# Optimization experiments

Measured on AMD Instinct MI355X. Metric: run time of the kernel, lower is better.

Reference implementation:

```python
import jax, jax.numpy as jnp
import numpy as np

E = 96   # embed dim (MultiheadAttention(96, 6))
H = 6    # heads
DH = E // H  # head dim = 16


def setup_inputs() -> dict:
    key = jax.random.key(0)
    ks = jax.random.split(key, 6)
    N, G = 4096, 64
    feats = jax.random.normal(ks[0], (N, E), jnp.float32)
    group = jax.random.randint(ks[1], (N,), 0, G)
    s = 1.0 / np.sqrt(E)
    # nn.MultiheadAttention packed in_proj [3E, E] and out_proj [E, E]
    w_in = jax.random.uniform(ks[2], (3 * E, E), jnp.float32, -s, s)
    b_in = jnp.zeros((3 * E,), jnp.float32)
    w_out = jax.random.uniform(ks[3], (E, E), jnp.float32, -s, s)
    b_out = jnp.zeros((E,), jnp.float32)
    # classifier Linear(96, 1)
    w_cls = jax.random.uniform(ks[4], (1, E), jnp.float32, -s, s)
    b_cls = jnp.zeros((1,), jnp.float32)
    return {"feats": feats, "group": group, "w_in": w_in, "b_in": b_in,
            "w_out": w_out, "b_out": b_out, "w_cls": w_cls, "b_cls": b_cls}


def reference(feats, group, w_in, b_in, w_out, b_out, w_cls, b_cls):
    # Per-group self-attention: softmax restricted to rows of the same group
    # is mathematically identical to running MHA on each group separately.
    N = feats.shape[0]
    qkv = feats @ w_in.T + b_in                     # [N, 3E]
    q, k, v = jnp.split(qkv, 3, axis=-1)            # each [N, E]
    to_heads = lambda t: t.reshape(N, H, DH).transpose(1, 0, 2)  # [H, N, DH]
    q = to_heads(q) * (1.0 / np.sqrt(DH))
    k = to_heads(k)
    v = to_heads(v)
    scores = jnp.einsum('hnd,hmd->hnm', q, k)       # [H, N, N]
    same_group = group[:, None] == group[None, :]   # [N, N] (diag always True)
    scores = jnp.where(same_group[None], scores, jnp.float32(-1e9))
    attn = jax.nn.softmax(scores, axis=-1)
    out = jnp.einsum('hnm,hmd->hnd', attn, v)       # [H, N, DH]
    out = out.transpose(1, 0, 2).reshape(N, E)
    out = out @ w_out.T + b_out                     # out_proj
    logits = out @ w_cls.T + b_cls                  # [N, 1]
    return jax.nn.sigmoid(logits)[:, 0]             # cluster_scores [N]
```

## Files before the change

### kernel.cpp

```cpp
#include <hip/hip_runtime.h>
#include <math.h>

#define N 4096
#define E 96
#define H 6
#define DH 16
#define G 64
#define CMAX 128
#define KSTR 19
#define FSTR 104
#define NW 8
#define NT 512

typedef __attribute__((ext_vector_type(8))) short short8;
typedef __attribute__((ext_vector_type(4))) float f32x4;

static __device__ __forceinline__ unsigned short f2bf(float f) {
    unsigned u = __builtin_bit_cast(unsigned, f);
    return (unsigned short)((u + 0x7fffu + ((u >> 16) & 1u)) >> 16);
}
static __device__ __forceinline__ unsigned pack2(float lo, float hi) {
    return (unsigned)f2bf(lo) | ((unsigned)f2bf(hi) << 16);
}

__global__ __launch_bounds__(NT, 4) void fused_kernel(const float* __restrict__ feats,
                                                      const int* __restrict__ grp,
                                                      const float* __restrict__ w_in,
                                                      const float* __restrict__ b_in,
                                                      const float* __restrict__ w_out,
                                                      const float* __restrict__ w_cls,
                                                      float* __restrict__ part) {
    __shared__ short fA[CMAX * FSTR];
    __shared__ short wB[48 * FSTR];
    __shared__ float bia[48];
    __shared__ float kh[CMAX * KSTR];
    __shared__ float vh[CMAX * KSTR];
    __shared__ float qh[CMAX * KSTR];
    __shared__ float ps[NW * 2 * CMAX];
    __shared__ int   bucket[CMAX];
    __shared__ unsigned long long smask[64];
    __shared__ int   scount[64];
    __shared__ int   soffs[64];
    __shared__ float wfh[DH];
    __shared__ int   scnt;

    int g = blockIdx.x & 63;
    int h = blockIdx.x >> 6;
    int tid = threadIdx.x, lane = tid & 63, wv = tid >> 6;

    #pragma unroll
    for (int c8 = 0; c8 < 8; ++c8) {
        int cc = wv * 8 + c8;
        bool mt = (grp[(cc << 6) + lane] == g);
        unsigned long long mask = __ballot(mt);
        if (lane == 0) { smask[cc] = mask; scount[cc] = __popcll(mask); }
    }

    if (tid < 384) {
        int row = tid >> 3, seg = tid & 7;
        int gcol = (row >> 4) * E + h * DH + (row & 15);
        const float4* src = (const float4*)(w_in + gcol * E + seg * 12);
        unsigned* dst = (unsigned*)(wB + row * FSTR + seg * 12);
        #pragma unroll
        for (int t = 0; t < 3; ++t) {
            float4 v = src[t];
            dst[2 * t]     = pack2(v.x, v.y);
            dst[2 * t + 1] = pack2(v.z, v.w);
        }
    } else if (tid < 432) {
        int c = tid - 384;
        bia[c] = b_in[(c >> 4) * E + h * DH + (c & 15)];
    } else if (wv == 7) {
        int dd = lane & 15, u4 = lane >> 4;
        float s = 0.f;
        for (int u = u4 * 24; u < u4 * 24 + 24; ++u)
            s += w_cls[u] * w_out[u * E + h * DH + dd];
        s += __shfl_xor(s, 16, 64);
        s += __shfl_xor(s, 32, 64);
        if (lane < DH) wfh[lane] = s;
    }
    __syncthreads();

    if (wv == 0) {
        int v = scount[lane];
        int x = v;
        #pragma unroll
        for (int o = 1; o < 64; o <<= 1) {
            int y = __shfl_up(x, o, 64);
            if (lane >= o) x += y;
        }
        soffs[lane] = x - v;
        if (lane == 63) scnt = x;
    } else {
        for (int idx = tid - 64; idx < CMAX * KSTR; idx += NT - 64) vh[idx] = 0.f;
    }
    __syncthreads();

    int cnt = scnt; if (cnt > CMAX) cnt = CMAX;

    #pragma unroll
    for (int c8 = 0; c8 < 8; ++c8) {
        int cc = wv * 8 + c8;
        unsigned long long mask = smask[cc];
        if ((mask >> lane) & 1ULL) {
            int pos = soffs[cc] + __popcll(mask & ((1ULL << lane) - 1ULL));
            if (pos < CMAX) bucket[pos] = (cc << 6) + lane;
        }
    }
    __syncthreads();

    {
        int srow = tid >> 2, sq = tid & 3;
        if (srow < cnt) {
            const float4* src = (const float4*)(feats + bucket[srow] * E + sq * 24);
            unsigned* dst = (unsigned*)(fA + srow * FSTR + sq * 24);
            #pragma unroll
            for (int t = 0; t < 6; ++t) {
                float4 v = src[t];
                dst[2 * t]     = pack2(v.x, v.y);
                dst[2 * t + 1] = pack2(v.z, v.w);
            }
        }
    }
    __syncthreads();

    {
        int lr = lane & 15, kg = lane >> 4;
        int njobs = ((cnt + 15) >> 4) * 3;
        for (int jj = wv; jj < njobs; jj += NW) {
            int rt = jj / 3;
            int ct = jj - rt * 3;
            const short* ab = fA + (rt * 16 + lr) * FSTR + kg * 8;
            const short* bb = wB + (ct * 16 + lr) * FSTR + kg * 8;
            f32x4 acc = {0.f, 0.f, 0.f, 0.f};
            acc = __builtin_amdgcn_mfma_f32_16x16x32_bf16(*(const short8*)(ab),
                                                          *(const short8*)(bb), acc, 0, 0, 0);
            acc = __builtin_amdgcn_mfma_f32_16x16x32_bf16(*(const short8*)(ab + 32),
                                                          *(const short8*)(bb + 32), acc, 0, 0, 0);
            acc = __builtin_amdgcn_mfma_f32_16x16x32_bf16(*(const short8*)(ab + 64),
                                                          *(const short8*)(bb + 64), acc, 0, 0, 0);
            float bias = bia[ct * 16 + lr];
            #pragma unroll
            for (int r = 0; r < 4; ++r) {
                int row = rt * 16 + kg * 4 + r;
                if (row < cnt) {
                    float v = acc[r] + bias;
                    if (ct == 1)      kh[row * KSTR + lr] = v;
                    else if (ct == 2) vh[row * KSTR + lr] = v;
                    else              qh[row * KSTR + lr] = v * 0.25f;
                }
            }
        }
    }
    __syncthreads();

    float* ps0 = ps + (2 * wv) * CMAX;
    float* ps1 = ps + (2 * wv + 1) * CMAX;
    for (int j0 = wv; j0 < cnt; j0 += 2 * NW) {
        int j1 = j0 + NW;
        bool has1 = (j1 < cnt);
        int j1r = has1 ? j1 : j0;

        float qv0[16], qv1[16];
        #pragma unroll
        for (int e = 0; e < 16; ++e) {
            qv0[e] = qh[j0 * KSTR + e];
            qv1[e] = qh[j1r * KSTR + e];
        }

        float a00 = 0.f, a10 = 0.f;
        #pragma unroll
        for (int e = 0; e < 16; ++e) {
            float kl = kh[lane * KSTR + e];
            a00 += qv0[e] * kl;
            a10 += qv1[e] * kl;
        }
        float s00 = (lane < cnt) ? a00 : -INFINITY;
        float s10 = (lane < cnt) ? a10 : -INFINITY;
        float s01 = -INFINITY, s11 = -INFINITY;
        if (cnt > 64) {
            float a01 = 0.f, a11 = 0.f;
            #pragma unroll
            for (int e = 0; e < 16; ++e) {
                float kl = kh[(64 + lane) * KSTR + e];
                a01 += qv0[e] * kl;
                a11 += qv1[e] * kl;
            }
            s01 = (64 + lane < cnt) ? a01 : -INFINITY;
            s11 = (64 + lane < cnt) ? a11 : -INFINITY;
        }

        float m0 = fmaxf(s00, s01), m1 = fmaxf(s10, s11);
        #pragma unroll
        for (int o = 32; o >= 1; o >>= 1) {
            m0 = fmaxf(m0, __shfl_xor(m0, o, 64));
            m1 = fmaxf(m1, __shfl_xor(m1, o, 64));
        }
        float p00 = __expf(s00 - m0), p10 = __expf(s10 - m1);
        float p01 = (cnt > 64) ? __expf(s01 - m0) : 0.f;
        float p11 = (cnt > 64) ? __expf(s11 - m1) : 0.f;
        float l0 = p00 + p01, l1 = p10 + p11;
        #pragma unroll
        for (int o = 32; o >= 1; o >>= 1) {
            l0 += __shfl_xor(l0, o, 64);
            l1 += __shfl_xor(l1, o, 64);
        }
        ps0[lane] = p00; ps0[64 + lane] = p01;
        ps1[lane] = p10; ps1[64 + lane] = p11;

        int mm4 = lane >> 4, dd = lane & 15;
        float acc0 = 0.f, acc1 = 0.f;
        #pragma unroll
        for (int k = 0; k < 16; ++k) {
            int m2 = mm4 + 4 * k;
            float vv = vh[m2 * KSTR + dd];
            acc0 += ps0[m2] * vv;
            acc1 += ps1[m2] * vv;
        }
        if (cnt > 64) {
            #pragma unroll
            for (int k = 16; k < 32; ++k) {
                int m2 = mm4 + 4 * k;
                float vv = vh[m2 * KSTR + dd];
                acc0 += ps0[m2] * vv;
                acc1 += ps1[m2] * vv;
            }
        }
        acc0 += __shfl_xor(acc0, 16, 64); acc1 += __shfl_xor(acc1, 16, 64);
        acc0 += __shfl_xor(acc0, 32, 64); acc1 += __shfl_xor(acc1, 32, 64);

        float pt0 = (acc0 / l0) * wfh[dd];
        float pt1 = (acc1 / l1) * wfh[dd];
        pt0 += __shfl_xor(pt0, 1, 64);  pt1 += __shfl_xor(pt1, 1, 64);
        pt0 += __shfl_xor(pt0, 2, 64);  pt1 += __shfl_xor(pt1, 2, 64);
        pt0 += __shfl_xor(pt0, 4, 64);  pt1 += __shfl_xor(pt1, 4, 64);
        pt0 += __shfl_xor(pt0, 8, 64);  pt1 += __shfl_xor(pt1, 8, 64);
        if (lane == 0) {
            part[bucket[j0] * 8 + h] = pt0;
            if (has1) part[bucket[j1] * 8 + h] = pt1;
        }
    }
}

__global__ __launch_bounds__(512) void sigmoid_kernel(const float* __restrict__ part,
                                                      const float* __restrict__ w_cls,
                                                      const float* __restrict__ b_out,
                                                      const float* __restrict__ b_cls,
                                                      float* __restrict__ out) {
    __shared__ float sbias;
    int tid = threadIdx.x;
    if (tid < 64) {
        float s = w_cls[tid] * b_out[tid];
        if (tid < 32) s += w_cls[tid + 64] * b_out[tid + 64];
        #pragma unroll
        for (int o = 32; o >= 1; o >>= 1) s += __shfl_xor(s, o, 64);
        if (tid == 0) sbias = s + b_cls[0];
    }
    __syncthreads();
    int i = blockIdx.x * 512 + tid;
    const float4* p = (const float4*)(part + i * 8);
    float4 u = p[0], v = p[1];
    float s = u.x + u.y + u.z + u.w + v.x + v.y + sbias;
    out[i] = 1.f / (1.f + __expf(-s));
}

extern "C" void kernel_launch(void* const* d_in, const int* in_sizes, int n_in,
                              void* d_out, int out_size, void* d_ws, size_t ws_size,
                              hipStream_t stream) {
    const float* feats = (const float*)d_in[0];
    const int*   grp   = (const int*)  d_in[1];
    const float* w_in  = (const float*)d_in[2];
    const float* b_in  = (const float*)d_in[3];
    const float* w_out = (const float*)d_in[4];
    const float* b_out = (const float*)d_in[5];
    const float* w_cls = (const float*)d_in[6];
    const float* b_cls = (const float*)d_in[7];
    float* out = (float*)d_out;

    float* part = (float*)d_ws;

    fused_kernel<<<G * H, NT, 0, stream>>>(feats, grp, w_in, b_in, w_out, w_cls, part);
    sigmoid_kernel<<<N / 512, 512, 0, stream>>>(part, w_cls, b_out, b_cls, out);
}
```

Before: 101.1 us.

## Split fused kernel into separate QKV projection and attention kernels

Moves group bucketing and the QKV projection into a new kernel launched once per (group, Q/K/V) pair, writing per-head Q/K/V tiles and group buckets to workspace. The attention kernel then only loads its head's precomputed tiles. Before, each of the 384 blocks scanned the group array, gathered features and re-did bucketing for its own head. The cost is an extra kernel launch and a global-memory round trip for Q/K/V, and the projection blocks read weights straight from global memory without staging them in shared memory.

After: 109.0 us. 1.08x slower.

```diff
diff --git a/kernel.cpp b/kernel.cpp
--- a/kernel.cpp
+++ b/kernel.cpp
@@ -14,6 +14,7 @@
 
 typedef __attribute__((ext_vector_type(8))) short short8;
 typedef __attribute__((ext_vector_type(4))) float f32x4;
+typedef __attribute__((ext_vector_type(4))) unsigned u32x4;
 
 static __device__ __forceinline__ unsigned short f2bf(float f) {
     unsigned u = __builtin_bit_cast(unsigned, f);
@@ -23,29 +24,24 @@
     return (unsigned)f2bf(lo) | ((unsigned)f2bf(hi) << 16);
 }
 
-__global__ __launch_bounds__(NT, 4) void fused_kernel(const float* __restrict__ feats,
-                                                      const int* __restrict__ grp,
-                                                      const float* __restrict__ w_in,
-                                                      const float* __restrict__ b_in,
-                                                      const float* __restrict__ w_out,
-                                                      const float* __restrict__ w_cls,
-                                                      float* __restrict__ part) {
+__global__ __launch_bounds__(NT, 4) void qkv_kernel(const float* __restrict__ feats,
+                                                    const int* __restrict__ grp,
+                                                    const float* __restrict__ w_in,
+                                                    const float* __restrict__ b_in,
+                                                    int* __restrict__ cnts,
+                                                    int* __restrict__ bucketg,
+                                                    float* __restrict__ Qc,
+                                                    float* __restrict__ Kc,
+                                                    float* __restrict__ Vc) {
     __shared__ short fA[CMAX * FSTR];
-    __shared__ short wB[48 * FSTR];
-    __shared__ float bia[48];
-    __shared__ float kh[CMAX * KSTR];
-    __shared__ float vh[CMAX * KSTR];
-    __shared__ float qh[CMAX * KSTR];
-    __shared__ float ps[NW * 2 * CMAX];
     __shared__ int   bucket[CMAX];
     __shared__ unsigned long long smask[64];
     __shared__ int   scount[64];
     __shared__ int   soffs[64];
-    __shared__ float wfh[DH];
     __shared__ int   scnt;
 
     int g = blockIdx.x & 63;
-    int h = blockIdx.x >> 6;
+    int p = blockIdx.x >> 6;
     int tid = threadIdx.x, lane = tid & 63, wv = tid >> 6;
 
     #pragma unroll
@@ -55,22 +51,108 @@
         unsigned long long mask = __ballot(mt);
         if (lane == 0) { smask[cc] = mask; scount[cc] = __popcll(mask); }
     }
-
-    if (tid < 384) {
-        int row = tid >> 3, seg = tid & 7;
-        int gcol = (row >> 4) * E + h * DH + (row & 15);
-        const float4* src = (const float4*)(w_in + gcol * E + seg * 12);
-        unsigned* dst = (unsigned*)(wB + row * FSTR + seg * 12);
-        #pragma unroll
-        for (int t = 0; t < 3; ++t) {
-            float4 v = src[t];
-            dst[2 * t]     = pack2(v.x, v.y);
-            dst[2 * t + 1] = pack2(v.z, v.w);
-        }
-    } else if (tid < 432) {
-        int c = tid - 384;
-        bia[c] = b_in[(c >> 4) * E + h * DH + (c & 15)];
-    } else if (wv == 7) {
+    __syncthreads();
+
+    if (wv == 0) {
+        int v = scount[lane];
+        int x = v;
+        #pragma unroll
+        for (int o = 1; o < 64; o <<= 1) {
+            int y = __shfl_up(x, o, 64);
+            if (lane >= o) x += y;
+        }
+        soffs[lane] = x - v;
+        if (lane == 63) scnt = x;
+    }
+    __syncthreads();
+
+    int cnt = scnt; if (cnt > CMAX) cnt = CMAX;
+
+    #pragma unroll
+    for (int c8 = 0; c8 < 8; ++c8) {
+        int cc = wv * 8 + c8;
+        unsigned long long mask = smask[cc];
+        if ((mask >> lane) & 1ULL) {
+            int pos = soffs[cc] + __popcll(mask & ((1ULL << lane) - 1ULL));
+            if (pos < CMAX) bucket[pos] = (cc << 6) + lane;
+        }
+    }
+    __syncthreads();
+
+    if (p == 0) {
+        if (tid == 0) cnts[g] = cnt;
+        if (tid < CMAX) bucketg[g * CMAX + tid] = bucket[tid];
+    }
+
+    {
+        int srow = tid >> 2, sq = tid & 3;
+        if (srow < cnt) {
+            const float4* src = (const float4*)(feats + bucket[srow] * E + sq * 24);
+            unsigned* dst = (unsigned*)(fA + srow * FSTR + sq * 24);
+            #pragma unroll
+            for (int t = 0; t < 6; ++t) {
+                float4 v = src[t];
+                dst[2 * t]     = pack2(v.x, v.y);
+                dst[2 * t + 1] = pack2(v.z, v.w);
+            }
+        }
+    }
+    __syncthreads();
+
+    int lr = lane & 15, kg = lane >> 4;
+    int rowtiles = (cnt + 15) >> 4;
+    int njobs = rowtiles * 6;
+    float* outb = (p == 0) ? Qc : (p == 1) ? Kc : Vc;
+    float scale = (p == 0) ? 0.25f : 1.0f;
+    #pragma unroll 1
+    for (int jj = wv; jj < njobs; jj += NW) {
+        int rt = jj / 6, ho = jj % 6;
+        int c = p * E + ho * DH + lr;
+        const float4* wr = (const float4*)(w_in + c * E);
+        const short* ab = fA + (rt * 16 + lr) * FSTR + kg * 8;
+        f32x4 acc = {0.f, 0.f, 0.f, 0.f};
+        #pragma unroll
+        for (int kc = 0; kc < 3; ++kc) {
+            float4 b0 = wr[kc * 8 + kg * 2];
+            float4 b1 = wr[kc * 8 + kg * 2 + 1];
+            u32x4 bw = { pack2(b0.x, b0.y), pack2(b0.z, b0.w),
+                         pack2(b1.x, b1.y), pack2(b1.z, b1.w) };
+            acc = __builtin_amdgcn_mfma_f32_16x16x32_bf16(*(const short8*)(ab + kc * 32),
+                    __builtin_bit_cast(short8, bw), acc, 0, 0, 0);
+        }
+        float bias = b_in[c];
+        float* ob = outb + ((ho * G + g) * CMAX) * 16;
+        #pragma unroll
+        for (int r = 0; r < 4; ++r) {
+            int row = rt * 16 + kg * 4 + r;
+            if (row < cnt) ob[row * 16 + lr] = (acc[r] + bias) * scale;
+        }
+    }
+}
+
+__global__ __launch_bounds__(NT, 4) void attn_kernel(const int* __restrict__ cnts,
+                                                     const int* __restrict__ bucketg,
+                                                     const float* __restrict__ Qc,
+                                                     const float* __restrict__ Kc,
+                                                     const float* __restrict__ Vc,
+                                                     const float* __restrict__ w_out,
+                                                     const float* __restrict__ w_cls,
+                                                     float* __restrict__ part) {
+    __shared__ float kh[CMAX * KSTR];
+    __shared__ float vh[CMAX * KSTR];
+    __shared__ float qh[CMAX * KSTR];
+    __shared__ float ps[NW * 2 * CMAX];
+    __shared__ int   sbk[CMAX];
+    __shared__ float wfh[DH];
+    __shared__ int   scnt_s;
+
+    int g = blockIdx.x & 63;
+    int h = blockIdx.x >> 6;
+    int tid = threadIdx.x, lane = tid & 63, wv = tid >> 6;
+
+    if (tid == 0) { int c = cnts[g]; scnt_s = (c > CMAX) ? CMAX : c; }
+    if (tid >= 64 && tid < 192) sbk[tid - 64] = bucketg[g * CMAX + (tid - 64)];
+    if (wv == 7) {
         int dd = lane & 15, u4 = lane >> 4;
         float s = 0.f;
         for (int u = u4 * 24; u < u4 * 24 + 24; ++u)
@@ -80,76 +162,24 @@
         if (lane < DH) wfh[lane] = s;
     }
     __syncthreads();
-
-    if (wv == 0) {
-        int v = scount[lane];
-        int x = v;
-        #pragma unroll
-        for (int o = 1; o < 64; o <<= 1) {
-            int y = __shfl_up(x, o, 64);
-            if (lane >= o) x += y;
-        }
-        soffs[lane] = x - v;
-        if (lane == 63) scnt = x;
-    } else {
-        for (int idx = tid - 64; idx < CMAX * KSTR; idx += NT - 64) vh[idx] = 0.f;
-    }
-    __syncthreads();
-
-    int cnt = scnt; if (cnt > CMAX) cnt = CMAX;
-
-    #pragma unroll
-    for (int c8 = 0; c8 < 8; ++c8) {
-        int cc = wv * 8 + c8;
-        unsigned long long mask = smask[cc];
-        if ((mask >> lane) & 1ULL) {
-            int pos = soffs[cc] + __popcll(mask & ((1ULL << lane) - 1ULL));
-            if (pos < CMAX) bucket[pos] = (cc << 6) + lane;
-        }
-    }
-    __syncthreads();
+    int cnt = scnt_s;
 
     {
-        int srow = tid >> 2, sq = tid & 3;
-        if (srow < cnt) {
-            const float4* src = (const float4*)(feats + bucket[srow] * E + sq * 24);
-            unsigned* dst = (unsigned*)(fA + srow * FSTR + sq * 24);
-            #pragma unroll
-            for (int t = 0; t < 6; ++t) {
-                float4 v = src[t];
-                dst[2 * t]     = pack2(v.x, v.y);
-                dst[2 * t + 1] = pack2(v.z, v.w);
+        int row = tid >> 2, q = tid & 3;
+        long base = ((long)(h * G + g) * CMAX + row) * 16 + q * 4;
+        if (row < cnt) {
+            float4 kv = *(const float4*)(Kc + base);
+            float4 vv = *(const float4*)(Vc + base);
+            float4 qv = *(const float4*)(Qc + base);
+            #pragma unroll
+            for (int t = 0; t < 4; ++t) {
+                kh[row * KSTR + q * 4 + t] = ((const float*)&kv)[t];
+                vh[row * KSTR + q * 4 + t] = ((const float*)&vv)[t];
+                qh[row * KSTR + q * 4 + t] = ((const float*)&qv)[t];
             }
-        }
-    }
-    __syncthreads();
-
-    {
-        int lr = lane & 15, kg = lane >> 4;
-        int njobs = ((cnt + 15) >> 4) * 3;
-        for (int jj = wv; jj < njobs; jj += NW) {
-            int rt = jj / 3;
-            int ct = jj - rt * 3;
-            const short* ab = fA + (rt * 16 + lr) * FSTR + kg * 8;
-            const short* bb = wB + (ct * 16 + lr) * FSTR + kg * 8;
-            f32x4 acc = {0.f, 0.f, 0.f, 0.f};
-            acc = __builtin_amdgcn_mfma_f32_16x16x32_bf16(*(const short8*)(ab),
-                                                          *(const short8*)(bb), acc, 0, 0, 0);
-            acc = __builtin_amdgcn_mfma_f32_16x16x32_bf16(*(const short8*)(ab + 32),
-                                                          *(const short8*)(bb + 32), acc, 0, 0, 0);
-            acc = __builtin_amdgcn_mfma_f32_16x16x32_bf16(*(const short8*)(ab + 64),
-                                                          *(const short8*)(bb + 64), acc, 0, 0, 0);
-            float bias = bia[ct * 16 + lr];
-            #pragma unroll
-            for (int r = 0; r < 4; ++r) {
-                int row = rt * 16 + kg * 4 + r;
-                if (row < cnt) {
-                    float v = acc[r] + bias;
-                    if (ct == 1)      kh[row * KSTR + lr] = v;
-                    else if (ct == 2) vh[row * KSTR + lr] = v;
-                    else              qh[row * KSTR + lr] = v * 0.25f;
-                }
-            }
+        } else {
+            #pragma unroll
+            for (int t = 0; t < 4; ++t) vh[row * KSTR + q * 4 + t] = 0.f;
         }
     }
     __syncthreads();
@@ -236,8 +266,8 @@
         pt0 += __shfl_xor(pt0, 4, 64);  pt1 += __shfl_xor(pt1, 4, 64);
         pt0 += __shfl_xor(pt0, 8, 64);  pt1 += __shfl_xor(pt1, 8, 64);
         if (lane == 0) {
-            part[bucket[j0] * 8 + h] = pt0;
-            if (has1) part[bucket[j1] * 8 + h] = pt1;
+            part[sbk[j0] * 8 + h] = pt0;
+            if (has1) part[sbk[j1] * 8 + h] = pt1;
         }
     }
 }
@@ -277,8 +307,14 @@
     const float* b_cls = (const float*)d_in[7];
     float* out = (float*)d_out;
 
-    float* part = (float*)d_ws;
-
-    fused_kernel<<<G * H, NT, 0, stream>>>(feats, grp, w_in, b_in, w_out, w_cls, part);
+    float* part   = (float*)d_ws;
+    int* cnts     = (int*)(part + N * 8);
+    int* bucketg  = cnts + 64;
+    float* Qc     = (float*)(bucketg + G * CMAX);
+    float* Kc     = Qc + H * G * CMAX * 16;
+    float* Vc     = Kc + H * G * CMAX * 16;
+
+    qkv_kernel<<<G * 3, NT, 0, stream>>>(feats, grp, w_in, b_in, cnts, bucketg, Qc, Kc, Vc);
+    attn_kernel<<<G * H, NT, 0, stream>>>(cnts, bucketg, Qc, Kc, Vc, w_out, w_cls, part);
     sigmoid_kernel<<<N / 512, 512, 0, stream>>>(part, w_cls, b_out, b_cls, out);
 }
```
